# Kernel optimization log

Measured on AMD Instinct MI355X. Metric: run time of the kernel, lower is better.

Reference implementation:

```python
import jax, jax.numpy as jnp
import numpy as np

DT = 0.01
KKT_REG = 1e-3  # small Tikhonov regularization for the all-active KKT proxy


def _forward(x, v, cld, dist, mu, cor, Minv):
    bs, n, d = x.shape  # d == 2
    nc = cld.shape[1]
    nd = n * d
    i, j = cld[..., 0], cld[..., 1]
    # contact point positions (n_p == 1 so object == point)
    p1 = jnp.take_along_axis(x, i[..., None], axis=1)  # [bs, nc, 2]
    p2 = jnp.take_along_axis(x, j[..., None], axis=1)
    diff = p2 - p1
    e_n = diff / jnp.linalg.norm(diff, axis=-1, keepdims=True)  # contact normal
    e_t = jnp.stack([-e_n[..., 1], e_n[..., 0]], axis=-1)       # tangent (d=2)
    # contact Jacobian [bs, nc, 2(normal/tangent), n, d]; c_tilde == 1 for n_p=1
    bi = jnp.arange(bs)[:, None]
    ci = jnp.arange(nc)[None, :]
    Jac = jnp.zeros((bs, nc, 2, n, d), x.dtype)
    Jac = Jac.at[bi, ci, 0, i].set(-e_n)
    Jac = Jac.at[bi, ci, 0, j].set(e_n)
    Jac = Jac.at[bi, ci, 1, i].set(-e_t)
    Jac = Jac.at[bi, ci, 1, j].set(e_t)
    J_cn = Jac[:, :, 0].reshape(bs, nc, nd)          # normal rows
    Jt = Jac[:, :, 1].reshape(bs, nc, nd)            # tangent rows
    # interleaved +/- tangent rows: J_ct[0::2]=Jt, J_ct[1::2]=-Jt
    J_ct = jnp.stack([Jt, -Jt], axis=2).reshape(bs, 2 * nc, nd)
    M = jnp.linalg.inv(Minv)
    pM = jnp.kron(M, jnp.eye(d, dtype=x.dtype))      # populated_M[i::d, i::d] = M
    E = jnp.kron(jnp.eye(nc, dtype=x.dtype), jnp.ones((2, 1), x.dtype))  # [2nc, nc]
    vflat = v.reshape(bs, nd)
    Mv = vflat @ pM.T
    Jcnv = jnp.einsum('bcj,bj->bc', J_cn, vflat)
    v_star0 = -dist / DT / 8.0
    h = jnp.concatenate([jnp.minimum(-v_star0, cor * Jcnv),
                         jnp.zeros((bs, 3 * nc), x.dtype)], axis=1)  # [bs, 4nc]
    G = jnp.concatenate([J_cn, J_ct, jnp.zeros((bs, nc, nd), x.dtype)], axis=1)
    m = 4 * nc
    F = jnp.zeros((bs, m, m), x.dtype)
    F = F.at[:, 3 * nc:, :nc].set(jax.vmap(jnp.diag)(mu))
    F = F.at[:, nc:3 * nc, 3 * nc:].set(E)
    F = F.at[:, 3 * nc:, nc:3 * nc].set(-E.T)
    # lcp_solver(pM, Mv, G, h, [], [], -F) replaced by the all-active KKT solve:
    #   [pM  G^T] [z]   [-Mv]
    #   [G   -F ] [l] = [-h ]
    K = jnp.zeros((bs, nd + m, nd + m), x.dtype)
    K = K.at[:, :nd, :nd].set(pM)
    K = K.at[:, :nd, nd:].set(jnp.swapaxes(G, 1, 2))
    K = K.at[:, nd:, :nd].set(G)
    K = K.at[:, nd:, nd:].set(-F)
    K = K + KKT_REG * jnp.eye(nd + m, dtype=x.dtype)
    rhs = jnp.concatenate([-Mv, -h], axis=1)
    sol = jnp.linalg.solve(K, rhs[..., None])[..., 0]
    v_plus = -sol[:, :nd]
    # torch.stack([x, new_v], 1).reshape(bs, -1)
    return jnp.concatenate([x.reshape(bs, nd), v_plus], axis=1)


def setup_inputs() -> dict:
    key = jax.random.key(0)
    ks = jax.random.split(key, 8)
    bs, n, nc = 1024, 64, 32
    x = jax.random.normal(ks[0], (bs, n, 2), jnp.float32)
    v = jax.random.normal(ks[1], (bs, n, 2), jnp.float32)
    i = jax.random.randint(ks[2], (bs, nc), 0, n // 2)
    j = jax.random.randint(ks[3], (bs, nc), n // 2, n)
    cld_ij_ids = jnp.stack([i, j], axis=-1).astype(jnp.int32)
    dist_ij = -0.1 * jax.random.uniform(ks[4], (bs, nc), jnp.float32)
    mu = jax.random.uniform(ks[5], (bs, nc), jnp.float32)
    cor = jax.random.uniform(ks[6], (bs, nc), jnp.float32)
    A = jax.random.normal(ks[7], (n, n), jnp.float32)
    Minv = A @ A.T / n + jnp.eye(n, dtype=jnp.float32)  # SPD inverse mass matrix
    return {"x": x, "v": v, "cld_ij_ids": cld_ij_ids, "dist_ij": dist_ij,
            "mu": mu, "cor": cor, "Minv": Minv}


def reference(x, v, cld_ij_ids, dist_ij, mu, cor, Minv):
    return _forward(x, v, cld_ij_ids, dist_ij, mu, cor, Minv)
```

## Files before the change

### kernel.cpp

```cpp
#include <hip/hip_runtime.h>
#include <math.h>


#define NBODY 64
#define NC    32
#define ND    128
#define EPS   1e-3f
#define WPAD  65

#define WAVE_SYNC() asm volatile("s_waitcnt lgkmcnt(0)" ::: "memory")

__device__ __forceinline__ float readlane_f(float x, int lane) {
  return __int_as_float(__builtin_amdgcn_readlane(__float_as_int(x), lane));
}

__global__ __launch_bounds__(64) void precompute_W(
    const float* __restrict__ Minv, float* __restrict__ Wg) {
  const int lane = threadIdx.x;
  const int col = blockIdx.x;

  float Mr[NBODY];
  const float4* mv = (const float4*)(Minv + lane * NBODY);
#pragma unroll
  for (int e4 = 0; e4 < 16; ++e4) {
    float4 t = mv[e4];
    Mr[4 * e4] = t.x; Mr[4 * e4 + 1] = t.y;
    Mr[4 * e4 + 2] = t.z; Mr[4 * e4 + 3] = t.w;
  }

  const float dlt = (lane == col) ? 1.0f : 0.0f;
  float s = dlt;
#pragma unroll
  for (int t = 0; t < 6; ++t) {
    float a0 = 0.f, a1 = 0.f, a2 = 0.f, a3 = 0.f;
#pragma unroll
    for (int e = 0; e < NBODY; e += 4) {
      a0 = fmaf(Mr[e],     readlane_f(s, e),     a0);
      a1 = fmaf(Mr[e + 1], readlane_f(s, e + 1), a1);
      a2 = fmaf(Mr[e + 2], readlane_f(s, e + 2), a2);
      a3 = fmaf(Mr[e + 3], readlane_f(s, e + 3), a3);
    }
    s = dlt - EPS * ((a0 + a1) + (a2 + a3));
  }
  float a0 = 0.f, a1 = 0.f, a2 = 0.f, a3 = 0.f;
#pragma unroll
  for (int e = 0; e < NBODY; e += 4) {
    a0 = fmaf(Mr[e],     readlane_f(s, e),     a0);
    a1 = fmaf(Mr[e + 1], readlane_f(s, e + 1), a1);
    a2 = fmaf(Mr[e + 2], readlane_f(s, e + 2), a2);
    a3 = fmaf(Mr[e + 3], readlane_f(s, e + 3), a3);
  }
  Wg[lane * NBODY + col] = (a0 + a1) + (a2 + a3);
}

__global__ __launch_bounds__(256, 1) void solve_batch(
    const float* __restrict__ x, const float* __restrict__ v,
    const int* __restrict__ cld, const float* __restrict__ dist,
    const float* __restrict__ cor, const float* __restrict__ Wg,
    float* __restrict__ out, int bs) {
  __shared__ float Wl[NBODY * WPAD];
  __shared__ float vL[4][ND];
  __shared__ float qL[4][ND];
  __shared__ float yL[4][ND];

  const int tid  = threadIdx.x;
  const int wave = tid >> 6;
  const int lane = tid & 63;
  const int b    = blockIdx.x * 4 + wave;

  for (int idx = tid; idx < NBODY * NBODY; idx += 256)
    Wl[(idx >> 6) * WPAD + (idx & 63)] = Wg[idx];
  __syncthreads();
  if (b >= bs) return;

  const float* xb = x + b * ND;
  const float* vb = v + b * ND;
  float* vw = vL[wave];
  float* qw = qL[wave];
  float* yw = yL[wave];

  vw[lane]      = vb[lane];
  vw[lane + 64] = vb[lane + 64];

  const int rc = lane & 31;
  const int myi = cld[b * 2 * NC + 2 * rc];
  const int myj = cld[b * 2 * NC + 2 * rc + 1];
  float dx = xb[2 * myj]     - xb[2 * myi];
  float dy = xb[2 * myj + 1] - xb[2 * myi + 1];
  float il = 1.0f / sqrtf(dx * dx + dy * dy);
  float enx = dx * il, eny = dy * il;
  float wx = (lane < 32) ? enx : -eny;
  float wy = (lane < 32) ? eny : enx;
  WAVE_SYNC();

  const int a1 = lane >> 1, kc = lane & 1;
  const float* W1 = Wl + a1 * WPAD;
  const float* W2 = Wl + (a1 + 32) * WPAD;
  {
    float s1 = 0.f, s2 = 0.f;
    for (int e = 0; e < NBODY; ++e) {
      float ve = vw[2 * e + kc];
      s1 = fmaf(W1[e], ve, s1);
      s2 = fmaf(W2[e], ve, s2);
    }
    qw[lane]      = vw[lane]      - EPS * s1;
    qw[lane + 64] = vw[lane + 64] - EPS * s2;
  }
  WAVE_SYNC();

  float rhs;
  {
    float qdx = qw[2 * myj]     - qw[2 * myi];
    float qdy = qw[2 * myj + 1] - qw[2 * myi + 1];
    float h = 0.0f;
    if (lane < 32) {
      float vdx = vw[2 * myj]     - vw[2 * myi];
      float vdy = vw[2 * myj + 1] - vw[2 * myi + 1];
      float jcnv = enx * vdx + eny * vdy;
      h = fminf(dist[b * NC + rc] * 12.5f, cor[b * NC + rc] * jcnv);
    }
    rhs = h - (wx * qdx + wy * qdy);
  }

  float row[64];
  const float* Wi = Wl + myi * WPAD;
  const float* Wj = Wl + myj * WPAD;
#pragma unroll
  for (int c = 0; c < 64; ++c) {
    int ic = __builtin_amdgcn_readlane(myi, c);
    int jc = __builtin_amdgcn_readlane(myj, c);
    float wcx = readlane_f(wx, c);
    float wcy = readlane_f(wy, c);
    float kap = (Wi[ic] - Wi[jc]) - (Wj[ic] - Wj[jc]);
    float a = (wx * wcx + wy * wcy) * kap;
    if (c == lane) a -= (lane < 32) ? EPS : 0.5f * EPS;
    row[c] = a;
  }

  float myinv = 0.0f;
#pragma unroll
  for (int k = 0; k < 64; ++k) {
    float pv = readlane_f(row[k], k);
    float r0 = 1.0f / pv;
    float m = (lane > k) ? row[k] * r0 : 0.0f;
    if (lane == k) myinv = r0;
    rhs = fmaf(-m, readlane_f(rhs, k), rhs);
#pragma unroll
    for (int c = k + 1; c < 64; ++c)
      row[c] = fmaf(-m, readlane_f(row[c], k), row[c]);
  }

  float myx = 0.0f;
  float xacc = rhs;
#pragma unroll
  for (int c = 63; c >= 0; --c) {
    float xc = readlane_f(xacc, c) * readlane_f(myinv, c);
    if (lane == c) myx = xc;
    xacc = fmaf(-row[c], xc, xacc);
  }

  {
    float y1 = 0.f, y2 = 0.f;
    const int b1 = a1, b2 = a1 + 32;
#pragma unroll
    for (int c = 0; c < 32; ++c) {
      int ic = __builtin_amdgcn_readlane(myi, c);
      int jc = __builtin_amdgcn_readlane(myj, c);
      float ex = readlane_f(wx, c),      ey = readlane_f(wy, c);
      float tx = readlane_f(wx, c + 32), ty = readlane_f(wy, c + 32);
      float lam = readlane_f(myx, c);
      float del = readlane_f(myx, c + 32);
      float wk = (kc ? ey : ex) * lam + (kc ? ty : tx) * del;
      y1 -= (ic == b1) ? wk : 0.0f;
      y2 += (jc == b2) ? wk : 0.0f;
    }
    yw[lane]      = y1;
    yw[lane + 64] = y2;
  }
  WAVE_SYNC();

  {
    float s1 = 0.f, s2 = 0.f;
    for (int e = 0; e < NBODY; ++e) {
      float ye = yw[2 * e + kc];
      s1 = fmaf(W1[e], ye, s1);
      s2 = fmaf(W2[e], ye, s2);
    }
    float* ob = out + b * 256;
    ob[lane]       = xb[lane];
    ob[lane + 64]  = xb[lane + 64];
    ob[128 + lane] = qw[lane] + s1;
    ob[192 + lane] = qw[lane + 64] + s2;
  }
}

extern "C" void kernel_launch(void* const* d_in, const int* in_sizes, int n_in,
                              void* d_out, int out_size, void* d_ws, size_t ws_size,
                              hipStream_t stream) {
  const float* x    = (const float*)d_in[0];
  const float* v    = (const float*)d_in[1];
  const int*   cld  = (const int*)  d_in[2];
  const float* dist = (const float*)d_in[3];
  const float* cor  = (const float*)d_in[5];
  const float* Minv = (const float*)d_in[6];
  float* out = (float*)d_out;

  const int bs = in_sizes[0] / ND;
  float* W = (float*)d_ws;

  precompute_W<<<NBODY, 64, 0, stream>>>(Minv, W);
  solve_batch<<<(bs + 3) / 4, 256, 0, stream>>>(x, v, cld, dist, cor, W, out, bs);
}
```

Baseline: 101.3 us.

## Split each batch element's 64x64 elimination across two waves

Each batch problem is now handled by a pair of waves instead of one. The Gaussian-elimination columns are split between the waves by column parity, which halves the per-lane register row. Multipliers are exchanged through shared memory with a block barrier at every pivot step. Back substitution is replaced by Gauss-Jordan style elimination of both the lower and upper parts, and the reciprocal uses a fast v_rcp instruction. The change targets register pressure and the serial per-wave work, at the cost of 64 block-wide barriers and the bounds check on bs being removed.

```diff
diff --git a/kernel.cpp b/kernel.cpp
--- a/kernel.cpp
+++ b/kernel.cpp
@@ -8,10 +8,14 @@
 #define EPS   1e-3f
 #define WPAD  65
 
-#define WAVE_SYNC() asm volatile("s_waitcnt lgkmcnt(0)" ::: "memory")
-
 __device__ __forceinline__ float readlane_f(float x, int lane) {
   return __int_as_float(__builtin_amdgcn_readlane(__float_as_int(x), lane));
+}
+
+__device__ __forceinline__ float rcp_fast(float x) {
+  float r;
+  asm("v_rcp_f32 %0, %1" : "=v"(r) : "v"(x));
+  return r;
 }
 
 __global__ __launch_bounds__(64) void precompute_W(
@@ -53,34 +57,39 @@
   Wg[lane * NBODY + col] = (a0 + a1) + (a2 + a3);
 }
 
-__global__ __launch_bounds__(256, 1) void solve_batch(
+__global__ __launch_bounds__(256, 2) void solve_batch(
     const float* __restrict__ x, const float* __restrict__ v,
     const int* __restrict__ cld, const float* __restrict__ dist,
     const float* __restrict__ cor, const float* __restrict__ Wg,
-    float* __restrict__ out, int bs) {
+    float* __restrict__ out) {
   __shared__ float Wl[NBODY * WPAD];
-  __shared__ float vL[4][ND];
-  __shared__ float qL[4][ND];
-  __shared__ float yL[4][ND];
+  __shared__ float vw_[2][ND];
+  __shared__ float qw_[2][ND];
+  __shared__ float yw_[2][ND];
+  __shared__ float mb_[2][2][64];
+  __shared__ float dv_[2][64];
 
   const int tid  = threadIdx.x;
   const int wave = tid >> 6;
   const int lane = tid & 63;
-  const int b    = blockIdx.x * 4 + wave;
+  const int pair = wave >> 1;
+  const int wp   = wave & 1;
+  const int b    = blockIdx.x * 2 + pair;
 
   for (int idx = tid; idx < NBODY * NBODY; idx += 256)
     Wl[(idx >> 6) * WPAD + (idx & 63)] = Wg[idx];
-  __syncthreads();
-  if (b >= bs) return;
 
   const float* xb = x + b * ND;
   const float* vb = v + b * ND;
-  float* vw = vL[wave];
-  float* qw = qL[wave];
-  float* yw = yL[wave];
-
-  vw[lane]      = vb[lane];
-  vw[lane + 64] = vb[lane + 64];
+  float* vw = vw_[pair];
+  float* qw = qw_[pair];
+  float* yw = yw_[pair];
+  float* mb0 = mb_[pair][0];
+  float* mb1 = mb_[pair][1];
+  float* dv = dv_[pair];
+
+  const int t = lane + 64 * wp;
+  vw[t] = vb[t];
 
   const int rc = lane & 31;
   const int myi = cld[b * 2 * NC + 2 * rc];
@@ -91,22 +100,17 @@
   float enx = dx * il, eny = dy * il;
   float wx = (lane < 32) ? enx : -eny;
   float wy = (lane < 32) ? eny : enx;
-  WAVE_SYNC();
-
-  const int a1 = lane >> 1, kc = lane & 1;
-  const float* W1 = Wl + a1 * WPAD;
-  const float* W2 = Wl + (a1 + 32) * WPAD;
-  {
-    float s1 = 0.f, s2 = 0.f;
-    for (int e = 0; e < NBODY; ++e) {
-      float ve = vw[2 * e + kc];
-      s1 = fmaf(W1[e], ve, s1);
-      s2 = fmaf(W2[e], ve, s2);
-    }
-    qw[lane]      = vw[lane]      - EPS * s1;
-    qw[lane + 64] = vw[lane + 64] - EPS * s2;
-  }
-  WAVE_SYNC();
+  __syncthreads();
+
+  const int kc = lane & 1;
+  const int a  = t >> 1;
+  const float* Wa = Wl + a * WPAD;
+  {
+    float s = 0.f;
+    for (int e = 0; e < NBODY; ++e) s = fmaf(Wa[e], vw[2 * e + kc], s);
+    qw[t] = vw[t] - EPS * s;
+  }
+  __syncthreads();
 
   float rhs;
   {
@@ -122,75 +126,70 @@
     rhs = h - (wx * qdx + wy * qdy);
   }
 
-  float row[64];
+  float rowh[32];
   const float* Wi = Wl + myi * WPAD;
   const float* Wj = Wl + myj * WPAD;
 #pragma unroll
-  for (int c = 0; c < 64; ++c) {
+  for (int tt = 0; tt < 32; ++tt) {
+    int c = 2 * tt + wp;
     int ic = __builtin_amdgcn_readlane(myi, c);
     int jc = __builtin_amdgcn_readlane(myj, c);
     float wcx = readlane_f(wx, c);
     float wcy = readlane_f(wy, c);
     float kap = (Wi[ic] - Wi[jc]) - (Wj[ic] - Wj[jc]);
-    float a = (wx * wcx + wy * wcy) * kap;
-    if (c == lane) a -= (lane < 32) ? EPS : 0.5f * EPS;
-    row[c] = a;
-  }
-
-  float myinv = 0.0f;
+    float aa = (wx * wcx + wy * wcy) * kap;
+    aa = (c == lane) ? aa - ((lane < 32) ? EPS : 0.5f * EPS) : aa;
+    rowh[tt] = aa;
+  }
+
 #pragma unroll
   for (int k = 0; k < 64; ++k) {
-    float pv = readlane_f(row[k], k);
-    float r0 = 1.0f / pv;
-    float m = (lane > k) ? row[k] * r0 : 0.0f;
-    if (lane == k) myinv = r0;
+    const int ow = k & 1;
+    float m;
+    if (wp == ow) {
+      float pv = readlane_f(rowh[k >> 1], k);
+      float r0 = rcp_fast(pv);
+      m = (lane == k) ? 0.0f : rowh[k >> 1] * r0;
+      (ow ? mb1 : mb0)[lane] = m;
+      if (lane == k) dv[k] = r0;
+    }
+    __syncthreads();
+    if (wp != ow) m = (ow ? mb1 : mb0)[lane];
     rhs = fmaf(-m, readlane_f(rhs, k), rhs);
 #pragma unroll
-    for (int c = k + 1; c < 64; ++c)
-      row[c] = fmaf(-m, readlane_f(row[c], k), row[c]);
-  }
-
-  float myx = 0.0f;
-  float xacc = rhs;
-#pragma unroll
-  for (int c = 63; c >= 0; --c) {
-    float xc = readlane_f(xacc, c) * readlane_f(myinv, c);
-    if (lane == c) myx = xc;
-    xacc = fmaf(-row[c], xc, xacc);
-  }
-
-  {
-    float y1 = 0.f, y2 = 0.f;
-    const int b1 = a1, b2 = a1 + 32;
+    for (int tt = (k >> 1); tt < 32; ++tt)
+      rowh[tt] = fmaf(-m, readlane_f(rowh[tt], k), rowh[tt]);
+  }
+
+  float myx = rhs * dv[lane];
+
+  {
+    float y = 0.f;
 #pragma unroll
     for (int c = 0; c < 32; ++c) {
-      int ic = __builtin_amdgcn_readlane(myi, c);
-      int jc = __builtin_amdgcn_readlane(myj, c);
       float ex = readlane_f(wx, c),      ey = readlane_f(wy, c);
       float tx = readlane_f(wx, c + 32), ty = readlane_f(wy, c + 32);
       float lam = readlane_f(myx, c);
       float del = readlane_f(myx, c + 32);
       float wk = (kc ? ey : ex) * lam + (kc ? ty : tx) * del;
-      y1 -= (ic == b1) ? wk : 0.0f;
-      y2 += (jc == b2) ? wk : 0.0f;
-    }
-    yw[lane]      = y1;
-    yw[lane + 64] = y2;
-  }
-  WAVE_SYNC();
-
-  {
-    float s1 = 0.f, s2 = 0.f;
-    for (int e = 0; e < NBODY; ++e) {
-      float ye = yw[2 * e + kc];
-      s1 = fmaf(W1[e], ye, s1);
-      s2 = fmaf(W2[e], ye, s2);
-    }
+      if (wp == 0) {
+        int ic = __builtin_amdgcn_readlane(myi, c);
+        y -= (ic == a) ? wk : 0.0f;
+      } else {
+        int jc = __builtin_amdgcn_readlane(myj, c);
+        y += (jc == a) ? wk : 0.0f;
+      }
+    }
+    yw[t] = y;
+  }
+  __syncthreads();
+
+  {
+    float s = 0.f;
+    for (int e = 0; e < NBODY; ++e) s = fmaf(Wa[e], yw[2 * e + kc], s);
     float* ob = out + b * 256;
-    ob[lane]       = xb[lane];
-    ob[lane + 64]  = xb[lane + 64];
-    ob[128 + lane] = qw[lane] + s1;
-    ob[192 + lane] = qw[lane + 64] + s2;
+    ob[t]       = xb[t];
+    ob[128 + t] = qw[t] + s;
   }
 }
 
@@ -209,5 +208,5 @@
   float* W = (float*)d_ws;
 
   precompute_W<<<NBODY, 64, 0, stream>>>(Minv, W);
-  solve_batch<<<(bs + 3) / 4, 256, 0, stream>>>(x, v, cld, dist, cor, W, out, bs);
-}
+  solve_batch<<<bs / 2, 256, 0, stream>>>(x, v, cld, dist, cor, W, out);
+}
```

After: 95.02 us. 6.2% less time.
